# Optimization experiments

Hardware: AMD Instinct MI355X
Metric: run time of the kernel (lower is better)

The kernel has to match this reference:

```python
import jax, jax.numpy as jnp
import numpy as np
from jax import lax

HEAD_DIM = 8          # attention_head_dim
EPS_ATTN = 1e-15
EPS_RMS = 1e-5
KPAD = 2              # kernel_size 5 -> padding 2


def setup_inputs() -> dict:
    key = jax.random.key(0)
    ks = jax.random.split(key, 9)
    B, C, H, W = 2, 1152, 64, 64
    inner = 1152                     # num_heads(144) * head_dim(8)
    ch3 = 3 * inner                  # 3456
    s = 0.02
    return {
        "hidden_states": jax.random.normal(ks[0], (B, C, H, W), jnp.float32),
        "Wq": jax.random.normal(ks[1], (inner, C), jnp.float32) * s,
        "Wk": jax.random.normal(ks[2], (inner, C), jnp.float32) * s,
        "Wv": jax.random.normal(ks[3], (inner, C), jnp.float32) * s,
        "proj_in_w": jax.random.normal(ks[4], (ch3, 1, 5, 5), jnp.float32) * s,   # depthwise 5x5
        "proj_out_w": jax.random.normal(ks[5], (ch3, HEAD_DIM, 1, 1), jnp.float32) * s,  # grouped 1x1, groups=3*heads
        "Wout": jax.random.normal(ks[6], (C, 2 * inner), jnp.float32) * s,
        "rms_w": jnp.ones((C,), jnp.float32),
        "rms_b": jnp.zeros((C,), jnp.float32),
    }


def reference(hidden_states, Wq, Wk, Wv, proj_in_w, proj_out_w, Wout, rms_w, rms_b):
    x = hidden_states
    B, C, H, W = x.shape
    xh = jnp.transpose(x, (0, 2, 3, 1))                      # BHWC
    q = xh @ Wq.T
    k = xh @ Wk.T
    v = xh @ Wv.T
    qkv = jnp.transpose(jnp.concatenate([q, k, v], axis=-1), (0, 3, 1, 2))  # B,3*inner,H,W
    ch = qkv.shape[1]
    # multiscale branch: depthwise 5x5 then grouped 1x1 (groups = 3*num_heads)
    ms = lax.conv_general_dilated(qkv, proj_in_w, (1, 1), [(KPAD, KPAD), (KPAD, KPAD)],
                                  dimension_numbers=("NCHW", "OIHW", "NCHW"),
                                  feature_group_count=ch)
    ms = lax.conv_general_dilated(ms, proj_out_w, (1, 1), [(0, 0), (0, 0)],
                                  dimension_numbers=("NCHW", "OIHW", "NCHW"),
                                  feature_group_count=ch // HEAD_DIM)
    hs = jnp.concatenate([qkv, ms], axis=1).astype(jnp.float32)   # B, 2*3*inner, H, W
    hs = hs.reshape(B, -1, 3 * HEAD_DIM, H * W)                   # B, G, 3d, N
    q2, k2, v2 = jnp.split(hs, 3, axis=2)                         # each B,G,d,N
    q2 = jax.nn.relu(q2)
    k2 = jax.nn.relu(k2)
    # linear attention: pad value with a ones row (for the normalizer)
    v_pad = jnp.concatenate([v2, jnp.ones_like(v2[:, :, :1])], axis=2)  # B,G,d+1,N
    scores = jnp.einsum("bgdn,bgen->bgde", v_pad, k2)             # B,G,d+1,d (tiny)
    out = jnp.einsum("bgde,bgen->bgdn", scores, q2)               # B,G,d+1,N
    out = out[:, :, :-1] / (out[:, :, -1:] + EPS_ATTN)            # normalize by last row
    out = out.reshape(B, -1, H, W)                                # B, 2*inner, H, W
    out = jnp.transpose(out, (0, 2, 3, 1)) @ Wout.T               # BHW,C_out
    # RMSNorm over channel (last) dim, with affine weight + bias
    ms2 = jnp.mean(out * out, axis=-1, keepdims=True)
    out = out * lax.rsqrt(ms2 + EPS_RMS) * rms_w + rms_b
    return jnp.transpose(out, (0, 3, 1, 2))
```

## Files before the change

kernel.cpp:

```cpp
#include <hip/hip_runtime.h>

typedef _Float16 f16;
typedef f16 f16x8 __attribute__((ext_vector_type(8)));
typedef float f32x16 __attribute__((ext_vector_type(16)));

#define NB 2
#define NC 1152
#define NHW 4096
#define NCH3 3456
#define NC2 2304

#define LO_SCALE 2048.0f
#define LO_INV (1.0f / 2048.0f)


__device__ __align__(16) f16 g_Wcat_h[(size_t)NCH3 * NC];
__device__ __align__(16) f16 g_Wcat_l[(size_t)NC * NC];
__device__ __align__(16) f16 g_WoutB_h[(size_t)NC * NC2];
__device__ __align__(16) f16 g_XT_h[(size_t)NB * NHW * NC];
__device__ __align__(16) f16 g_XT_l[(size_t)NB * NHW * NC];
__device__ __align__(16) f16 g_qkv[(size_t)NB * NCH3 * NHW];
__device__ __align__(16) f16 g_ms[(size_t)NB * NCH3 * NHW];
__device__ __align__(16) f16 g_attnT_h[(size_t)NB * NHW * NC2];
__device__ float g_part[NB * NHW];

__device__ __forceinline__ void gload16(const void* g, void* l) {
  __builtin_amdgcn_global_load_lds(
      (const __attribute__((address_space(1))) unsigned int*)g,
      (__attribute__((address_space(3))) unsigned int*)l, 16, 0, 0);
}

__device__ __forceinline__ void split_f16(float v, f16& h, f16& l) {
  h = (f16)v;
  l = (f16)((v - (float)h) * LO_SCALE);
}

__global__ __launch_bounds__(256) void convert_weights(
    const float* __restrict__ wq, const float* __restrict__ wk,
    const float* __restrict__ wv, const float* __restrict__ wout) {
  size_t idx = ((size_t)blockIdx.x * 256 + threadIdx.x) * 4;
  const size_t NWC = (size_t)NCH3 * NC;
  const size_t NWO = (size_t)NC * NC2;
  if (idx < NWC) {
    int p = (int)(idx / NC);
    int kk = (int)(idx % NC);
    int role = p / 1152, w = p % 1152;
    int g = w >> 3, r = w & 7;
    int c = g * 24 + role * 8 + r;
    const float* src = (c < 1152) ? wq + (size_t)c * NC + kk
                      : (c < 2304) ? wk + (size_t)(c - 1152) * NC + kk
                                   : wv + (size_t)(c - 2304) * NC + kk;
    if (p < 1152) {
#pragma unroll
      for (int j = 0; j < 4; ++j)
        split_f16(src[j], g_Wcat_h[idx + j], g_Wcat_l[idx + j]);
    } else {
#pragma unroll
      for (int j = 0; j < 4; ++j) g_Wcat_h[idx + j] = (f16)src[j];
    }
  } else {
    size_t k = idx - NWC;
    if (k < NWO) {
      const float* src = wout + k;
#pragma unroll
      for (int j = 0; j < 4; ++j) g_WoutB_h[k + j] = (f16)src[j];
    }
  }
}

__global__ __launch_bounds__(256) void transpose_x(const float* __restrict__ x) {
  __shared__ float tile[32][33];
  int z = blockIdx.z;
  int p0 = blockIdx.x * 32, c0 = blockIdx.y * 32;
  int tx = threadIdx.x, ty = threadIdx.y;
#pragma unroll
  for (int i = 0; i < 32; i += 8)
    tile[ty + i][tx] = x[((size_t)z * NC + c0 + ty + i) * NHW + p0 + tx];
  __syncthreads();
#pragma unroll
  for (int i = 0; i < 32; i += 8) {
    size_t o = ((size_t)z * NHW + p0 + ty + i) * NC + c0 + tx;
    split_f16(tile[tx][ty + i], g_XT_h[o], g_XT_l[o]);
  }
}

__device__ __forceinline__ void gemm1_split_deep(char* smem, int bm, int bn, int bz) {
  const int tid = threadIdx.x;
  const int lane = tid & 63;
  const int wid = tid >> 6;
  const int wr = wid >> 2, wc = wid & 3;
  const size_t boff = (size_t)bz * ((size_t)NHW * NC);
  const f16* Bh = g_XT_h + boff;
  const f16* Bl = g_XT_l + boff;
  f16* Cb = g_qkv + (size_t)bz * ((size_t)NCH3 * NHW);
  const int srow = tid >> 2;
  const int skb = (((tid & 3) ^ ((srow >> 1) & 3)) * 8);
  const f16* gAh = g_Wcat_h + (size_t)(bm + srow) * NC + skb;
  const f16* gAl = g_Wcat_l + (size_t)(bm + srow) * NC + skb;
  const f16* gBh0 = Bh + (size_t)(bn + srow) * NC + skb;
  const f16* gBl0 = Bl + (size_t)(bn + srow) * NC + skb;
  const f16* gBh1 = Bh + (size_t)(bn + 128 + srow) * NC + skb;
  const f16* gBl1 = Bl + (size_t)(bn + 128 + srow) * NC + skb;
  const int ldso = tid * 16;

  f32x16 acc[2][2] = {};
  f32x16 acc2[2][2] = {};
  const int r31 = lane & 31;
  const int key = (r31 >> 1) & 3;
  const int kblk = lane >> 5;

#define BUFS(b, off) (smem + (b) * 49152 + (off))
#define STG_S0(buf, tile)                                       \
  do {                                                          \
    size_t ko = (size_t)(tile) * 32;                            \
    gload16(gAh + ko, BUFS(buf, 0) + ldso);                     \
    gload16(gAl + ko, BUFS(buf, 8192) + ldso);                  \
    gload16(gBh0 + ko, BUFS(buf, 16384) + ldso);                \
  } while (0)
#define STG_S1(buf, tile)                                       \
  do {                                                          \
    size_t ko = (size_t)(tile) * 32;                            \
    gload16(gBh1 + ko, BUFS(buf, 24576) + ldso);                \
    gload16(gBl0 + ko, BUFS(buf, 32768) + ldso);                \
    gload16(gBl1 + ko, BUFS(buf, 40960) + ldso);                \
  } while (0)

#define FPH_S(buf, kh, STG)                                                    \
  do {                                                                         \
    STG;                                                                       \
    const int bsw = (((kh) * 2 + kblk) ^ key) * 8;                             \
    const f16* sAh = (const f16*)BUFS(buf, 0);                                 \
    const f16* sAl = (const f16*)BUFS(buf, 8192);                              \
    const f16* sBh = (const f16*)BUFS(buf, 16384);                             \
    const f16* sBl = (const f16*)BUFS(buf, 32768);                             \
    f16x8 ah[2], al[2], bh[2], bl[2];                                          \
    _Pragma("unroll") for (int mb = 0; mb < 2; ++mb) {                         \
      int ro = (wr * 64 + mb * 32 + r31) * 32 + bsw;                           \
      ah[mb] = *(const f16x8*)(sAh + ro);                                      \
      al[mb] = *(const f16x8*)(sAl + ro);                                      \
    }                                                                          \
    _Pragma("unroll") for (int nb = 0; nb < 2; ++nb) {                         \
      int ro = (wc * 64 + nb * 32 + r31) * 32 + bsw;                           \
      bh[nb] = *(const f16x8*)(sBh + ro);                                      \
      bl[nb] = *(const f16x8*)(sBl + ro);                                      \
    }                                                                          \
    __builtin_amdgcn_s_setprio(1);                                             \
    _Pragma("unroll") for (int mb = 0; mb < 2; ++mb)                           \
      _Pragma("unroll") for (int nb = 0; nb < 2; ++nb) {                       \
        acc[mb][nb]  = __builtin_amdgcn_mfma_f32_32x32x16_f16(ah[mb], bh[nb], acc[mb][nb], 0, 0, 0);  \
        acc2[mb][nb] = __builtin_amdgcn_mfma_f32_32x32x16_f16(ah[mb], bl[nb], acc2[mb][nb], 0, 0, 0); \
        acc2[mb][nb] = __builtin_amdgcn_mfma_f32_32x32x16_f16(al[mb], bh[nb], acc2[mb][nb], 0, 0, 0); \
      }                                                                        \
    __builtin_amdgcn_s_setprio(0);                                             \
  } while (0)

  const int NT = NC / 32;
  STG_S0(0, 0); STG_S1(0, 0);
  STG_S0(1, 1); STG_S1(1, 1);
  int cb = 0;
#pragma unroll 1
  for (int t = 0; t < NT - 2; ++t) {
    asm volatile("s_waitcnt vmcnt(6)" ::: "memory");
    __builtin_amdgcn_s_barrier();
    int pb = cb + 2; if (pb >= 3) pb -= 3;
    FPH_S(cb, 0, STG_S0(pb, t + 2));
    FPH_S(cb, 1, STG_S1(pb, t + 2));
    cb = (cb == 2) ? 0 : cb + 1;
  }
  asm volatile("s_waitcnt vmcnt(6)" ::: "memory");
  __builtin_amdgcn_s_barrier();
  FPH_S(cb, 0, (void)0);
  FPH_S(cb, 1, (void)0);
  cb = (cb == 2) ? 0 : cb + 1;
  asm volatile("s_waitcnt vmcnt(0)" ::: "memory");
  __builtin_amdgcn_s_barrier();
  FPH_S(cb, 0, (void)0);
  FPH_S(cb, 1, (void)0);
#undef STG_S0
#undef STG_S1
#undef FPH_S
#undef BUFS
#pragma unroll
  for (int mb = 0; mb < 2; ++mb)
#pragma unroll
    for (int nb = 0; nb < 2; ++nb) {
      int col = bn + wc * 64 + nb * 32 + r31;
#pragma unroll
      for (int reg = 0; reg < 16; ++reg) {
        int row = bm + wr * 64 + mb * 32 + (reg & 3) + 8 * (reg >> 2) + 4 * (lane >> 5);
        Cb[(size_t)row * NHW + col] = (f16)(acc[mb][nb][reg] + acc2[mb][nb][reg] * LO_INV);
      }
    }
}

__device__ __forceinline__ void gemm1_plain_deep(char* smem, int bmG, int bn, int bz) {
  f16* sA0 = (f16*)smem;
  f16* sB0 = (f16*)(smem + 49152);
  const int tid = threadIdx.x;
  const int lane = tid & 63;
  const int wid = tid >> 6;
  const int wr = wid >> 2, wc = wid & 3;
  const f16* Bb = g_XT_h + (size_t)bz * ((size_t)NHW * NC);
  f16* Cb = g_qkv + (size_t)bz * ((size_t)NCH3 * NHW);
  const int srow = tid >> 2;
  const int skb = (((tid & 3) ^ ((srow >> 1) & 3)) * 8);
  const f16* gA0 = g_Wcat_h + (size_t)(bmG + srow) * NC + skb;
  const f16* gA1 = g_Wcat_h + (size_t)(bmG + 128 + srow) * NC + skb;
  const f16* gB0 = Bb + (size_t)(bn + srow) * NC + skb;
  const f16* gB1 = Bb + (size_t)(bn + 128 + srow) * NC + skb;
  const int ldso = tid * 16;

  f32x16 acc[4][2] = {};
  const int r31 = lane & 31;
  const int key = (r31 >> 1) & 3;
  const int kblk = lane >> 5;

#define SA(b) (sA0 + (b) * 8192)
#define SB(b) (sB0 + (b) * 8192)
#define STG_A(buf, tile)                                        \
  do {                                                          \
    size_t ko = (size_t)(tile) * 32;                            \
    gload16(gA0 + ko, (char*)SA(buf) + ldso);                   \
    gload16(gA1 + ko, (char*)SA(buf) + 8192 + ldso);            \
  } while (0)
#define STG_B(buf, tile)                                        \
  do {                                                          \
    size_t ko = (size_t)(tile) * 32;                            \
    gload16(gB0 + ko, (char*)SB(buf) + ldso);                   \
    gload16(gB1 + ko, (char*)SB(buf) + 8192 + ldso);            \
  } while (0)
#define FPH_P(buf, ks, STG)                                                    \
  do {                                                                         \
    STG;                                                                       \
    const int bsw = (((ks) * 2 + kblk) ^ key) * 8;                             \
    f16x8 af[4], bf[2];                                                        \
    _Pragma("unroll") for (int ma = 0; ma < 4; ++ma) {                         \
      int row = wr * 128 + ma * 32 + r31;                                      \
      af[ma] = *(const f16x8*)(SA(buf) + row * 32 + bsw);                      \
    }                                                                          \
    _Pragma("unroll") for (int nb = 0; nb < 2; ++nb) {                         \
      int row = wc * 64 + nb * 32 + r31;                                       \
      bf[nb] = *(const f16x8*)(SB(buf) + row * 32 + bsw);                      \
    }                                                                          \
    __builtin_amdgcn_s_setprio(1);                                             \
    _Pragma("unroll") for (int ma = 0; ma < 4; ++ma)                           \
      _Pragma("unroll") for (int nb = 0; nb < 2; ++nb)                         \
        acc[ma][nb] = __builtin_amdgcn_mfma_f32_32x32x16_f16(af[ma], bf[nb], acc[ma][nb], 0, 0, 0); \
    __builtin_amdgcn_s_setprio(0);                                             \
  } while (0)

  const int NT = NC / 32;
  STG_A(0, 0); STG_B(0, 0);
  STG_A(1, 1); STG_B(1, 1);
  int cb = 0;
#pragma unroll 1
  for (int t = 0; t < NT - 2; ++t) {
    asm volatile("s_waitcnt vmcnt(4)" ::: "memory");
    __builtin_amdgcn_s_barrier();
    int pb = cb + 2; if (pb >= 3) pb -= 3;
    FPH_P(cb, 0, STG_A(pb, t + 2));
    FPH_P(cb, 1, STG_B(pb, t + 2));
    cb = (cb == 2) ? 0 : cb + 1;
  }
  asm volatile("s_waitcnt vmcnt(4)" ::: "memory");
  __builtin_amdgcn_s_barrier();
  FPH_P(cb, 0, (void)0);
  FPH_P(cb, 1, (void)0);
  cb = (cb == 2) ? 0 : cb + 1;
  asm volatile("s_waitcnt vmcnt(0)" ::: "memory");
  __builtin_amdgcn_s_barrier();
  FPH_P(cb, 0, (void)0);
  FPH_P(cb, 1, (void)0);
#undef STG_A
#undef STG_B
#undef FPH_P
#undef SA
#undef SB
#pragma unroll
  for (int ma = 0; ma < 4; ++ma)
#pragma unroll
    for (int nb = 0; nb < 2; ++nb) {
      int col = bn + wc * 64 + nb * 32 + r31;
#pragma unroll
      for (int reg = 0; reg < 16; ++reg) {
        int row = bmG + wr * 128 + ma * 32 + (reg & 3) + 8 * (reg >> 2) + 4 * (lane >> 5);
        Cb[(size_t)row * NHW + col] = (f16)acc[ma][nb][reg];
      }
    }
}

__global__ __launch_bounds__(512, 1) void gemm1_kernel() {
  __shared__ __align__(16) char smem[147456];
  int bid = blockIdx.x;
  int swz = (bid & 7) * 72 + (bid >> 3);
  if (swz < 288) {
    int bx = swz % 9, rem = swz / 9;
    gemm1_split_deep(smem, bx * 128, (rem & 15) * 256, rem >> 4);
  } else {
    int w2 = swz - 288;
    int bx = w2 % 9, rem = w2 / 9;
    gemm1_plain_deep(smem, 1152 + bx * 256, (rem & 15) * 256, rem >> 4);
  }
}

__global__ __launch_bounds__(256, 2) void gemm2_kernel(float* __restrict__ out) {
  __shared__ __align__(16) f16 sA[3][128 * 32];
  __shared__ __align__(16) f16 sB[3][128 * 32];
  int bid = blockIdx.x;
  int swz = (bid & 7) * (576 / 8) + (bid >> 3);
  int bx = swz % 9, rem = swz / 9;
  int bm = bx * 128, bn = (rem & 31) * 128, bz = rem >> 5;

  const int tid = threadIdx.x;
  const int lane = tid & 63;
  const int wid = tid >> 6;
  const int wr = wid >> 1, wc = wid & 1;
  const f16* Bb = g_attnT_h + (size_t)bz * ((size_t)NHW * NC2);
  float* Cb = out + (size_t)bz * ((size_t)NC * NHW);
  const int srow = tid >> 2;
  const int skb = (((tid & 3) ^ ((srow >> 1) & 3)) * 8);
  const f16* gA0 = g_WoutB_h + (size_t)(bm + srow) * NC2 + skb;
  const f16* gA1 = g_WoutB_h + (size_t)(bm + 64 + srow) * NC2 + skb;
  const f16* gB0 = Bb + (size_t)(bn + srow) * NC2 + skb;
  const f16* gB1 = Bb + (size_t)(bn + 64 + srow) * NC2 + skb;
  const int ldso = tid * 16;

  f32x16 acc[2][2] = {};
  const int r31 = lane & 31;
  const int key = (r31 >> 1) & 3;
  const int kblk = lane >> 5;

#define STG_A2(buf, tile)                               \
  do {                                                  \
    size_t ko = (size_t)(tile) * 32;                    \
    gload16(gA0 + ko, (char*)sA[buf] + ldso);           \
    gload16(gA1 + ko, (char*)sA[buf] + 4096 + ldso);    \
  } while (0)
#define STG_B2(buf, tile)                               \
  do {                                                  \
    size_t ko = (size_t)(tile) * 32;                    \
    gload16(gB0 + ko, (char*)sB[buf] + ldso);           \
    gload16(gB1 + ko, (char*)sB[buf] + 4096 + ldso);    \
  } while (0)
#define FPH_2(buf, ks, STG)                                                    \
  do {                                                                         \
    STG;                                                                       \
    const int bsw = (((ks) * 2 + kblk) ^ key) * 8;                             \
    f16x8 af[2], bf[2];                                                        \
    _Pragma("unroll") for (int mb = 0; mb < 2; ++mb)                           \
      af[mb] = *(const f16x8*)(sA[buf] + (wr * 64 + mb * 32 + r31) * 32 + bsw);\
    _Pragma("unroll") for (int nb = 0; nb < 2; ++nb)                           \
      bf[nb] = *(const f16x8*)(sB[buf] + (wc * 64 + nb * 32 + r31) * 32 + bsw);\
    __builtin_amdgcn_s_setprio(1);                                             \
    _Pragma("unroll") for (int mb = 0; mb < 2; ++mb)                           \
      _Pragma("unroll") for (int nb = 0; nb < 2; ++nb)                         \
        acc[mb][nb] = __builtin_amdgcn_mfma_f32_32x32x16_f16(af[mb], bf[nb], acc[mb][nb], 0, 0, 0); \
    __builtin_amdgcn_s_setprio(0);                                             \
  } while (0)

  const int NT = NC2 / 32;
  STG_A2(0, 0); STG_B2(0, 0);
  STG_A2(1, 1); STG_B2(1, 1);
  int cb = 0;
#pragma unroll 1
  for (int t = 0; t < NT - 2; ++t) {
    asm volatile("s_waitcnt vmcnt(4)" ::: "memory");
    __builtin_amdgcn_s_barrier();
    int pb = cb + 2; if (pb >= 3) pb -= 3;
    FPH_2(cb, 0, STG_A2(pb, t + 2));
    FPH_2(cb, 1, STG_B2(pb, t + 2));
    cb = (cb == 2) ? 0 : cb + 1;
  }
  asm volatile("s_waitcnt vmcnt(4)" ::: "memory");
  __builtin_amdgcn_s_barrier();
  FPH_2(cb, 0, (void)0);
  FPH_2(cb, 1, (void)0);
  cb = (cb == 2) ? 0 : cb + 1;
  asm volatile("s_waitcnt vmcnt(0)" ::: "memory");
  __builtin_amdgcn_s_barrier();
  FPH_2(cb, 0, (void)0);
  FPH_2(cb, 1, (void)0);
#undef STG_A2
#undef STG_B2
#undef FPH_2
#pragma unroll
  for (int nb = 0; nb < 2; ++nb) {
    int col = bn + wc * 64 + nb * 32 + r31;
    float csum = 0.f;
#pragma unroll
    for (int mb = 0; mb < 2; ++mb)
#pragma unroll
      for (int reg = 0; reg < 16; ++reg) {
        int row = bm + wr * 64 + mb * 32 + (reg & 3) + 8 * (reg >> 2) + 4 * (lane >> 5);
        float v = acc[mb][nb][reg];
        Cb[(size_t)row * NHW + col] = v;
        csum += v * v;
      }
    atomicAdd(&g_part[bz * NHW + col], csum);
  }
}

__global__ __launch_bounds__(256) void conv_kernel(const float* __restrict__ wdw,
                                                   const float* __restrict__ wpw) {
  const int z = blockIdx.z, gg = blockIdx.y;
  const int pbase = (gg % 3) * 1152 + (gg / 3) * 8;
  const int px = blockIdx.x * 2048 + threadIdx.x * 8;
  const int h = px >> 6, w0 = px & 63;
  const f16* base = g_qkv + ((size_t)z * NCH3 + pbase) * NHW;

  float dw[8][8];
#pragma unroll
  for (int ci = 0; ci < 8; ++ci) {
    const float* wd = wdw + (gg * 8 + ci) * 25;
    const f16* srcc = base + (size_t)ci * NHW;
    float acc[8] = {};
#pragma unroll
    for (int dy = -2; dy <= 2; ++dy) {
      int hh = h + dy;
      if (hh < 0 || hh > 63) continue;
      const f16* row = srcc + hh * 64;
      f16x8 Lv = {}, Rv = {};
      if (w0 >= 8) Lv = *(const f16x8*)(row + w0 - 8);
      f16x8 Mv = *(const f16x8*)(row + w0);
      if (w0 <= 48) Rv = *(const f16x8*)(row + w0 + 8);
      float c[24];
#pragma unroll
      for (int i = 0; i < 8; ++i) {
        c[i] = (float)Lv[i];
        c[8 + i] = (float)Mv[i];
        c[16 + i] = (float)Rv[i];
      }
      const float* wrow = wd + (dy + 2) * 5;
#pragma unroll
      for (int dx = 0; dx < 5; ++dx) {
        float wv = wrow[dx];
#pragma unroll
        for (int j = 0; j < 8; ++j) acc[j] += c[6 + j + dx] * wv;
      }
    }
#pragma unroll
    for (int j = 0; j < 8; ++j) dw[ci][j] = acc[j];
  }
#pragma unroll
  for (int o = 0; o < 8; ++o) {
    const float* wp = wpw + (size_t)(gg * 8 + o) * 8;
    float out[8] = {};
#pragma unroll
    for (int i = 0; i < 8; ++i) {
      float wv = wp[i];
#pragma unroll
      for (int j = 0; j < 8; ++j) out[j] += wv * dw[i][j];
    }
    f16x8 ov;
#pragma unroll
    for (int j = 0; j < 8; ++j) ov[j] = (f16)out[j];
    *(f16x8*)(g_ms + ((size_t)z * NCH3 + pbase + o) * NHW + px) = ov;
  }
}

__global__ __launch_bounds__(256) void attn_kernel() {
  int g = blockIdx.x;
  int z = blockIdx.y;
  int tid = threadIdx.x;
  const f16* buf = (g < 144) ? g_qkv : g_ms;
  int gq = (g < 144) ? g : g - 144;
  const f16* qp = buf + ((size_t)z * NCH3 + gq * 8) * NHW;
  const f16* kp = buf + ((size_t)z * NCH3 + 1152 + gq * 8) * NHW;
  const f16* vp = buf + ((size_t)z * NCH3 + 2304 + gq * 8) * NHW;

  float s[9][8];
#pragma unroll
  for (int d = 0; d < 9; ++d)
#pragma unroll
    for (int e = 0; e < 8; ++e) s[d][e] = 0.f;

  for (int p0 = tid * 8; p0 < NHW; p0 += 2048) {
    f16x8 kx[8], vx[8];
#pragma unroll
    for (int e = 0; e < 8; ++e) kx[e] = *(const f16x8*)(kp + (size_t)e * NHW + p0);
#pragma unroll
    for (int d = 0; d < 8; ++d) vx[d] = *(const f16x8*)(vp + (size_t)d * NHW + p0);
#pragma unroll
    for (int j = 0; j < 8; ++j) {
      float kv[8], vv[8];
#pragma unroll
      for (int e = 0; e < 8; ++e) kv[e] = fmaxf((float)kx[e][j], 0.f);
#pragma unroll
      for (int d = 0; d < 8; ++d) vv[d] = (float)vx[d][j];
#pragma unroll
      for (int e = 0; e < 8; ++e) {
#pragma unroll
        for (int d = 0; d < 8; ++d) s[d][e] += vv[d] * kv[e];
        s[8][e] += kv[e];
      }
    }
  }
#pragma unroll
  for (int d = 0; d < 9; ++d)
#pragma unroll
    for (int e = 0; e < 8; ++e) {
      float v = s[d][e];
#pragma unroll
      for (int off = 32; off > 0; off >>= 1) v += __shfl_xor(v, off, 64);
      s[d][e] = v;
    }
  __shared__ float sred[4][72];
  __shared__ float sc[72];
  int w = tid >> 6, lane = tid & 63;
  if (lane == 0) {
#pragma unroll
    for (int d = 0; d < 9; ++d)
#pragma unroll
      for (int e = 0; e < 8; ++e) sred[w][d * 8 + e] = s[d][e];
  }
  __syncthreads();
  if (tid < 72) sc[tid] = sred[0][tid] + sred[1][tid] + sred[2][tid] + sred[3][tid];
  __syncthreads();
  float scl[9][8];
#pragma unroll
  for (int d = 0; d < 9; ++d)
#pragma unroll
    for (int e = 0; e < 8; ++e) scl[d][e] = sc[d * 8 + e];

  for (int p0 = tid * 8; p0 < NHW; p0 += 2048) {
    f16x8 qx[8];
#pragma unroll
    for (int e = 0; e < 8; ++e) qx[e] = *(const f16x8*)(qp + (size_t)e * NHW + p0);
#pragma unroll
    for (int j = 0; j < 8; ++j) {
      float qv[8];
#pragma unroll
      for (int e = 0; e < 8; ++e) qv[e] = fmaxf((float)qx[e][j], 0.f);
      float o[9];
#pragma unroll
      for (int d = 0; d < 9; ++d) {
        float a = 0.f;
#pragma unroll
        for (int e = 0; e < 8; ++e) a += scl[d][e] * qv[e];
        o[d] = a;
      }
      float r = 1.f / (o[8] + 1e-15f);
      f16x8 oh;
#pragma unroll
      for (int d = 0; d < 8; ++d) oh[d] = (f16)(o[d] * r);
      *(f16x8*)(g_attnT_h + ((size_t)z * NHW + p0 + j) * NC2 + g * 8) = oh;
    }
  }
}

__global__ __launch_bounds__(256) void rms_zero() {
  g_part[blockIdx.x * 256 + threadIdx.x] = 0.f;
}
__global__ __launch_bounds__(256) void rms_norm(float* __restrict__ y,
                                                const float* __restrict__ w,
                                                const float* __restrict__ b) {
  size_t i = ((size_t)blockIdx.x * 256 + threadIdx.x) * 4;
  float4 v = *(const float4*)(y + i);
  int p = (int)(i & (NHW - 1));
  int c = (int)((i >> 12) % NC);
  int z = (int)(i / ((size_t)NC * NHW));
  const float inv = 1.0f / NC;
  float wc = w[c], bc = b[c];
  const float* pp = &g_part[z * NHW + p];
  v.x = v.x * rsqrtf(pp[0] * inv + 1e-5f) * wc + bc;
  v.y = v.y * rsqrtf(pp[1] * inv + 1e-5f) * wc + bc;
  v.z = v.z * rsqrtf(pp[2] * inv + 1e-5f) * wc + bc;
  v.w = v.w * rsqrtf(pp[3] * inv + 1e-5f) * wc + bc;
  *(float4*)(y + i) = v;
}

extern "C" void kernel_launch(void* const* d_in, const int* in_sizes, int n_in,
                              void* d_out, int out_size, void* d_ws, size_t ws_size,
                              hipStream_t stream) {
  const float* x = (const float*)d_in[0];
  const float* wq = (const float*)d_in[1];
  const float* wk = (const float*)d_in[2];
  const float* wv = (const float*)d_in[3];
  const float* wdw = (const float*)d_in[4];
  const float* wpw = (const float*)d_in[5];
  const float* wout = (const float*)d_in[6];
  const float* rw = (const float*)d_in[7];
  const float* rb = (const float*)d_in[8];
  float* y = (float*)d_out;

  convert_weights<<<6480, 256, 0, stream>>>(wq, wk, wv, wout);
  transpose_x<<<dim3(128, 36, 2), dim3(32, 8), 0, stream>>>(x);
  gemm1_kernel<<<576, 512, 0, stream>>>();
  conv_kernel<<<dim3(2, 432, 2), 256, 0, stream>>>(wdw, wpw);
  attn_kernel<<<dim3(288, 2), 256, 0, stream>>>();
  rms_zero<<<32, 256, 0, stream>>>();
  gemm2_kernel<<<576, 256, 0, stream>>>(y);
  rms_norm<<<9216, 256, 0, stream>>>(y, rw, rb);
}
```

Measured before the change: 438.1 us.

## Shrink K/V gemm1 tiles, interleave block classes, restructure gemm2 pipeline

The K/V part of gemm1 now uses 128x256 tiles instead of 256x256, and the grid grows to 864 blocks. Blocks are interleaved so one split (hi/lo) Q block alternates with two K/V blocks, which balances work across CUs. gemm2 is refactored into a templated body that issues all stage loads at once, computes both k-halves after one barrier, and adds sched_barriers plus a trailing barrier per iteration. The aim is better load balance and occupancy, at the cost of lower per-block data reuse in the K/V GEMM and an extra barrier per K-step in gemm2.

```diff
diff --git a/kernel.cpp b/kernel.cpp
--- a/kernel.cpp
+++ b/kernel.cpp
@@ -193,9 +193,9 @@
     }
 }
 
-__device__ __forceinline__ void gemm1_plain_deep(char* smem, int bmG, int bn, int bz) {
+__device__ __forceinline__ void gemm1_kv_deep(char* smem, int bmG, int bn, int bz) {
   f16* sA0 = (f16*)smem;
-  f16* sB0 = (f16*)(smem + 49152);
+  f16* sB0 = (f16*)(smem + 24576);
   const int tid = threadIdx.x;
   const int lane = tid & 63;
   const int wid = tid >> 6;
@@ -205,86 +205,79 @@
   const int srow = tid >> 2;
   const int skb = (((tid & 3) ^ ((srow >> 1) & 3)) * 8);
   const f16* gA0 = g_Wcat_h + (size_t)(bmG + srow) * NC + skb;
-  const f16* gA1 = g_Wcat_h + (size_t)(bmG + 128 + srow) * NC + skb;
   const f16* gB0 = Bb + (size_t)(bn + srow) * NC + skb;
   const f16* gB1 = Bb + (size_t)(bn + 128 + srow) * NC + skb;
   const int ldso = tid * 16;
 
-  f32x16 acc[4][2] = {};
+  f32x16 acc[2][2] = {};
   const int r31 = lane & 31;
   const int key = (r31 >> 1) & 3;
   const int kblk = lane >> 5;
 
-#define SA(b) (sA0 + (b) * 8192)
+#define SA(b) (sA0 + (b) * 4096)
 #define SB(b) (sB0 + (b) * 8192)
-#define STG_A(buf, tile)                                        \
+#define STG_KV(buf, tile)                                       \
   do {                                                          \
     size_t ko = (size_t)(tile) * 32;                            \
     gload16(gA0 + ko, (char*)SA(buf) + ldso);                   \
-    gload16(gA1 + ko, (char*)SA(buf) + 8192 + ldso);            \
-  } while (0)
-#define STG_B(buf, tile)                                        \
-  do {                                                          \
-    size_t ko = (size_t)(tile) * 32;                            \
     gload16(gB0 + ko, (char*)SB(buf) + ldso);                   \
     gload16(gB1 + ko, (char*)SB(buf) + 8192 + ldso);            \
   } while (0)
-#define FPH_P(buf, ks, STG)                                                    \
+#define FPH_KV(buf, ks, STG)                                                   \
   do {                                                                         \
     STG;                                                                       \
     const int bsw = (((ks) * 2 + kblk) ^ key) * 8;                             \
-    f16x8 af[4], bf[2];                                                        \
-    _Pragma("unroll") for (int ma = 0; ma < 4; ++ma) {                         \
-      int row = wr * 128 + ma * 32 + r31;                                      \
-      af[ma] = *(const f16x8*)(SA(buf) + row * 32 + bsw);                      \
+    f16x8 af[2], bf[2];                                                        \
+    _Pragma("unroll") for (int mb = 0; mb < 2; ++mb) {                         \
+      int row = wr * 64 + mb * 32 + r31;                                       \
+      af[mb] = *(const f16x8*)(SA(buf) + row * 32 + bsw);                      \
     }                                                                          \
     _Pragma("unroll") for (int nb = 0; nb < 2; ++nb) {                         \
       int row = wc * 64 + nb * 32 + r31;                                       \
       bf[nb] = *(const f16x8*)(SB(buf) + row * 32 + bsw);                      \
     }                                                                          \
     __builtin_amdgcn_s_setprio(1);                                             \
-    _Pragma("unroll") for (int ma = 0; ma < 4; ++ma)                           \
+    _Pragma("unroll") for (int mb = 0; mb < 2; ++mb)                           \
       _Pragma("unroll") for (int nb = 0; nb < 2; ++nb)                         \
-        acc[ma][nb] = __builtin_amdgcn_mfma_f32_32x32x16_f16(af[ma], bf[nb], acc[ma][nb], 0, 0, 0); \
+        acc[mb][nb] = __builtin_amdgcn_mfma_f32_32x32x16_f16(af[mb], bf[nb], acc[mb][nb], 0, 0, 0); \
     __builtin_amdgcn_s_setprio(0);                                             \
   } while (0)
 
   const int NT = NC / 32;
-  STG_A(0, 0); STG_B(0, 0);
-  STG_A(1, 1); STG_B(1, 1);
+  STG_KV(0, 0);
+  STG_KV(1, 1);
   int cb = 0;
 #pragma unroll 1
   for (int t = 0; t < NT - 2; ++t) {
-    asm volatile("s_waitcnt vmcnt(4)" ::: "memory");
+    asm volatile("s_waitcnt vmcnt(3)" ::: "memory");
     __builtin_amdgcn_s_barrier();
     int pb = cb + 2; if (pb >= 3) pb -= 3;
-    FPH_P(cb, 0, STG_A(pb, t + 2));
-    FPH_P(cb, 1, STG_B(pb, t + 2));
+    FPH_KV(cb, 0, STG_KV(pb, t + 2));
+    FPH_KV(cb, 1, (void)0);
     cb = (cb == 2) ? 0 : cb + 1;
   }
-  asm volatile("s_waitcnt vmcnt(4)" ::: "memory");
+  asm volatile("s_waitcnt vmcnt(3)" ::: "memory");
   __builtin_amdgcn_s_barrier();
-  FPH_P(cb, 0, (void)0);
-  FPH_P(cb, 1, (void)0);
+  FPH_KV(cb, 0, (void)0);
+  FPH_KV(cb, 1, (void)0);
   cb = (cb == 2) ? 0 : cb + 1;
   asm volatile("s_waitcnt vmcnt(0)" ::: "memory");
   __builtin_amdgcn_s_barrier();
-  FPH_P(cb, 0, (void)0);
-  FPH_P(cb, 1, (void)0);
-#undef STG_A
-#undef STG_B
-#undef FPH_P
+  FPH_KV(cb, 0, (void)0);
+  FPH_KV(cb, 1, (void)0);
+#undef STG_KV
+#undef FPH_KV
 #undef SA
 #undef SB
 #pragma unroll
-  for (int ma = 0; ma < 4; ++ma)
+  for (int mb = 0; mb < 2; ++mb)
 #pragma unroll
     for (int nb = 0; nb < 2; ++nb) {
       int col = bn + wc * 64 + nb * 32 + r31;
 #pragma unroll
       for (int reg = 0; reg < 16; ++reg) {
-        int row = bmG + wr * 128 + ma * 32 + (reg & 3) + 8 * (reg >> 2) + 4 * (lane >> 5);
-        Cb[(size_t)row * NHW + col] = (f16)acc[ma][nb][reg];
+        int row = bmG + wr * 64 + mb * 32 + (reg & 3) + 8 * (reg >> 2) + 4 * (lane >> 5);
+        Cb[(size_t)row * NHW + col] = (f16)acc[mb][nb][reg];
       }
     }
 }
@@ -292,37 +285,36 @@
 __global__ __launch_bounds__(512, 1) void gemm1_kernel() {
   __shared__ __align__(16) char smem[147456];
   int bid = blockIdx.x;
-  int swz = (bid & 7) * 72 + (bid >> 3);
-  if (swz < 288) {
-    int bx = swz % 9, rem = swz / 9;
+  int cls = bid % 3;
+  int base = bid / 3;
+  if (cls == 0) {
+    int bx = base % 9, rem = base / 9;
     gemm1_split_deep(smem, bx * 128, (rem & 15) * 256, rem >> 4);
   } else {
-    int w2 = swz - 288;
-    int bx = w2 % 9, rem = w2 / 9;
-    gemm1_plain_deep(smem, 1152 + bx * 256, (rem & 15) * 256, rem >> 4);
-  }
-}
-
-__global__ __launch_bounds__(256, 2) void gemm2_kernel(float* __restrict__ out) {
+    int k = base * 2 + (cls - 1);
+    int bx = k % 18, rem = k / 18;
+    gemm1_kv_deep(smem, 1152 + bx * 128, (rem & 15) * 256, rem >> 4);
+  }
+}
+
+template <int M, int N, int K>
+__device__ __forceinline__ void gemm_body_plain(
+    const f16* __restrict__ A, const f16* __restrict__ Bt,
+    float* __restrict__ C, int bm, int bn, int bz) {
   __shared__ __align__(16) f16 sA[3][128 * 32];
   __shared__ __align__(16) f16 sB[3][128 * 32];
-  int bid = blockIdx.x;
-  int swz = (bid & 7) * (576 / 8) + (bid >> 3);
-  int bx = swz % 9, rem = swz / 9;
-  int bm = bx * 128, bn = (rem & 31) * 128, bz = rem >> 5;
-
   const int tid = threadIdx.x;
   const int lane = tid & 63;
   const int wid = tid >> 6;
   const int wr = wid >> 1, wc = wid & 1;
-  const f16* Bb = g_attnT_h + (size_t)bz * ((size_t)NHW * NC2);
-  float* Cb = out + (size_t)bz * ((size_t)NC * NHW);
+  const f16* Bb = Bt + (size_t)bz * ((size_t)N * K);
+  float* Cb = C + (size_t)bz * ((size_t)M * N);
   const int srow = tid >> 2;
   const int skb = (((tid & 3) ^ ((srow >> 1) & 3)) * 8);
-  const f16* gA0 = g_WoutB_h + (size_t)(bm + srow) * NC2 + skb;
-  const f16* gA1 = g_WoutB_h + (size_t)(bm + 64 + srow) * NC2 + skb;
-  const f16* gB0 = Bb + (size_t)(bn + srow) * NC2 + skb;
-  const f16* gB1 = Bb + (size_t)(bn + 64 + srow) * NC2 + skb;
+  const f16* gA0 = A + (size_t)(bm + srow) * K + skb;
+  const f16* gA1 = A + (size_t)(bm + 64 + srow) * K + skb;
+  const f16* gB0 = Bb + (size_t)(bn + srow) * K + skb;
+  const f16* gB1 = Bb + (size_t)(bn + 64 + srow) * K + skb;
   const int ldso = tid * 16;
 
   f32x16 acc[2][2] = {};
@@ -330,59 +322,54 @@
   const int key = (r31 >> 1) & 3;
   const int kblk = lane >> 5;
 
-#define STG_A2(buf, tile)                               \
+#define STAGE_P(buf, tile)                              \
   do {                                                  \
     size_t ko = (size_t)(tile) * 32;                    \
     gload16(gA0 + ko, (char*)sA[buf] + ldso);           \
     gload16(gA1 + ko, (char*)sA[buf] + 4096 + ldso);    \
-  } while (0)
-#define STG_B2(buf, tile)                               \
-  do {                                                  \
-    size_t ko = (size_t)(tile) * 32;                    \
     gload16(gB0 + ko, (char*)sB[buf] + ldso);           \
     gload16(gB1 + ko, (char*)sB[buf] + 4096 + ldso);    \
   } while (0)
-#define FPH_2(buf, ks, STG)                                                    \
+
+#define COMPUTE_P(buf)                                                         \
   do {                                                                         \
-    STG;                                                                       \
-    const int bsw = (((ks) * 2 + kblk) ^ key) * 8;                             \
-    f16x8 af[2], bf[2];                                                        \
-    _Pragma("unroll") for (int mb = 0; mb < 2; ++mb)                           \
-      af[mb] = *(const f16x8*)(sA[buf] + (wr * 64 + mb * 32 + r31) * 32 + bsw);\
-    _Pragma("unroll") for (int nb = 0; nb < 2; ++nb)                           \
-      bf[nb] = *(const f16x8*)(sB[buf] + (wc * 64 + nb * 32 + r31) * 32 + bsw);\
-    __builtin_amdgcn_s_setprio(1);                                             \
-    _Pragma("unroll") for (int mb = 0; mb < 2; ++mb)                           \
+    _Pragma("unroll") for (int kh = 0; kh < 2; ++kh) {                         \
+      const int bsw = ((kh * 2 + kblk) ^ key) * 8;                             \
+      f16x8 af[2], bf[2];                                                      \
+      _Pragma("unroll") for (int mb = 0; mb < 2; ++mb)                         \
+        af[mb] = *(const f16x8*)(sA[buf] + (wr * 64 + mb * 32 + r31) * 32 + bsw); \
       _Pragma("unroll") for (int nb = 0; nb < 2; ++nb)                         \
-        acc[mb][nb] = __builtin_amdgcn_mfma_f32_32x32x16_f16(af[mb], bf[nb], acc[mb][nb], 0, 0, 0); \
-    __builtin_amdgcn_s_setprio(0);                                             \
-  } while (0)
-
-  const int NT = NC2 / 32;
-  STG_A2(0, 0); STG_B2(0, 0);
-  STG_A2(1, 1); STG_B2(1, 1);
-  int cb = 0;
+        bf[nb] = *(const f16x8*)(sB[buf] + (wc * 64 + nb * 32 + r31) * 32 + bsw); \
+      __builtin_amdgcn_s_setprio(1);                                           \
+      _Pragma("unroll") for (int mb = 0; mb < 2; ++mb)                         \
+        _Pragma("unroll") for (int nb = 0; nb < 2; ++nb)                       \
+          acc[mb][nb] = __builtin_amdgcn_mfma_f32_32x32x16_f16(af[mb], bf[nb], acc[mb][nb], 0, 0, 0); \
+      __builtin_amdgcn_s_setprio(0);                                           \
+    }                                                                          \
+  } while (0)
+
+  const int NT = K / 32;
+  STAGE_P(0, 0);
+  STAGE_P(1, 1);
+  int cb = 0, sb = 2;
 #pragma unroll 1
-  for (int t = 0; t < NT - 2; ++t) {
+  for (int t = 0; t < NT - 1; ++t) {
     asm volatile("s_waitcnt vmcnt(4)" ::: "memory");
     __builtin_amdgcn_s_barrier();
-    int pb = cb + 2; if (pb >= 3) pb -= 3;
-    FPH_2(cb, 0, STG_A2(pb, t + 2));
-    FPH_2(cb, 1, STG_B2(pb, t + 2));
+    __builtin_amdgcn_sched_barrier(0);
+    if (t + 2 < NT) STAGE_P(sb, t + 2);
+    COMPUTE_P(cb);
+    __builtin_amdgcn_sched_barrier(0);
+    __builtin_amdgcn_s_barrier();
     cb = (cb == 2) ? 0 : cb + 1;
-  }
-  asm volatile("s_waitcnt vmcnt(4)" ::: "memory");
-  __builtin_amdgcn_s_barrier();
-  FPH_2(cb, 0, (void)0);
-  FPH_2(cb, 1, (void)0);
-  cb = (cb == 2) ? 0 : cb + 1;
+    sb = (sb == 2) ? 0 : sb + 1;
+  }
   asm volatile("s_waitcnt vmcnt(0)" ::: "memory");
   __builtin_amdgcn_s_barrier();
-  FPH_2(cb, 0, (void)0);
-  FPH_2(cb, 1, (void)0);
-#undef STG_A2
-#undef STG_B2
-#undef FPH_2
+  __builtin_amdgcn_sched_barrier(0);
+  COMPUTE_P(cb);
+#undef STAGE_P
+#undef COMPUTE_P
 #pragma unroll
   for (int nb = 0; nb < 2; ++nb) {
     int col = bn + wc * 64 + nb * 32 + r31;
@@ -393,11 +380,20 @@
       for (int reg = 0; reg < 16; ++reg) {
         int row = bm + wr * 64 + mb * 32 + (reg & 3) + 8 * (reg >> 2) + 4 * (lane >> 5);
         float v = acc[mb][nb][reg];
-        Cb[(size_t)row * NHW + col] = v;
+        Cb[(size_t)row * N + col] = v;
         csum += v * v;
       }
     atomicAdd(&g_part[bz * NHW + col], csum);
   }
+}
+
+__global__ __launch_bounds__(256, 2) void gemm2_kernel(float* __restrict__ out) {
+  int bid = blockIdx.x;
+  int swz = (bid & 7) * (576 / 8) + (bid >> 3);
+  int bx = swz % 9, rem = swz / 9;
+  int by = rem & 31, bz = rem >> 5;
+  gemm_body_plain<NC, NHW, NC2>(g_WoutB_h, g_attnT_h, out,
+                                bx * 128, by * 128, bz);
 }
 
 __global__ __launch_bounds__(256) void conv_kernel(const float* __restrict__ wdw,
@@ -585,7 +581,7 @@
 
   convert_weights<<<6480, 256, 0, stream>>>(wq, wk, wv, wout);
   transpose_x<<<dim3(128, 36, 2), dim3(32, 8), 0, stream>>>(x);
-  gemm1_kernel<<<576, 512, 0, stream>>>();
+  gemm1_kernel<<<864, 512, 0, stream>>>();
   conv_kernel<<<dim3(2, 432, 2), 256, 0, stream>>>(wdw, wpw);
   attn_kernel<<<dim3(288, 2), 256, 0, stream>>>();
   rms_zero<<<32, 256, 0, stream>>>();
```

Measured after the change: 432.7 us. Within noise of the previous version (-1.2%).
